# Performance work log

Measured on AMD Instinct MI355X. Metric: run time of the kernel, lower is better.

Reference implementation:

```python
import jax, jax.numpy as jnp
import numpy as np

N = 524288
EPS = 1e-5

def _ln(x, g, b):
    m = jnp.mean(x, axis=-1, keepdims=True)
    v = jnp.mean((x - m) ** 2, axis=-1, keepdims=True)
    return (x - m) * jax.lax.rsqrt(v + EPS) * g + b

def _blk(x, w1, g, b, w2, b2):
    # Linear(no bias) -> LayerNorm -> ReLU -> Linear(bias)
    return jax.nn.relu(_ln(x @ w1, g, b)) @ w2 + b2

def _lin_init(k, fin, fout):
    return jax.random.normal(k, (fin, fout), dtype=jnp.float32) * (1.0 / np.sqrt(fin))

def setup_inputs() -> dict:
    key = jax.random.key(0)
    ks = jax.random.split(key, 16)
    d = {
        'representation_128': jax.random.normal(ks[0], (N, 128), dtype=jnp.float32),
        'grasp_pose': jax.random.normal(ks[1], (N, 6), dtype=jnp.float32),
        'opening': jax.random.uniform(ks[2], (N, 1), dtype=jnp.float32),
        # key branch: 128 -> 64 (no bias) -> LN -> ReLU -> 32
        'kw1': _lin_init(ks[3], 128, 64), 'kg': jnp.ones(64), 'kb': jnp.zeros(64),
        'kw2': _lin_init(ks[4], 64, 32), 'kb2': jnp.zeros(32),
        # query branch: 6 -> 16 -> 32
        'qw1': _lin_init(ks[5], 6, 16), 'qg': jnp.ones(16), 'qb': jnp.zeros(16),
        'qw2': _lin_init(ks[6], 16, 32), 'qb2': jnp.zeros(32),
        # value branch: 1 -> 16 -> 32
        'vw1': _lin_init(ks[7], 1, 16), 'vg': jnp.ones(16), 'vb': jnp.zeros(16),
        'vw2': _lin_init(ks[8], 16, 32), 'vb2': jnp.zeros(32),
        # attention head: 32 -> 32 -> 16
        'aw1': _lin_init(ks[9], 32, 32), 'ag': jnp.ones(32), 'ab': jnp.zeros(32),
        'aw2': _lin_init(ks[10], 32, 16), 'ab2': jnp.zeros(16),
        # residuals: 135 -> 64 -> 32 -> 16 (two LN blocks, final Linear with bias)
        'rw1': _lin_init(ks[11], 135, 64), 'rg1': jnp.ones(64), 'rb1': jnp.zeros(64),
        'rw2': _lin_init(ks[12], 64, 32), 'rg2': jnp.ones(32), 'rb2': jnp.zeros(32),
        'rw3': _lin_init(ks[13], 32, 16), 'rb3': jnp.zeros(16),
        # get_value: 32 -> 16 -> 1
        'gw1': _lin_init(ks[14], 32, 16), 'gg': jnp.ones(16), 'gb': jnp.zeros(16),
        'gw2': _lin_init(ks[15], 16, 1), 'gb2': jnp.zeros(1),
    }
    return d

def reference(representation_128, grasp_pose, opening,
              kw1, kg, kb, kw2, kb2,
              qw1, qg, qb, qw2, qb2,
              vw1, vg, vb, vw2, vb2,
              aw1, ag, ab, aw2, ab2,
              rw1, rg1, rb1, rw2, rg2, rb2, rw3, rb3,
              gw1, gg, gb, gw2, gb2):
    # residual path on concat([rep, pose, opening]) -> [N,135]
    res_in = jnp.concatenate([representation_128, grasp_pose, opening], axis=-1)
    h = jax.nn.relu(_ln(res_in @ rw1, rg1, rb1))
    h = jax.nn.relu(_ln(h @ rw2, rg2, rb2))
    residuals = h @ rw3 + rb3                       # [N,16]
    key = _blk(representation_128, kw1, kg, kb, kw2, kb2)   # [N,32]
    query = _blk(grasp_pose, qw1, qg, qb, qw2, qb2)          # [N,32]
    value = _blk(opening, vw1, vg, vb, vw2, vb2)             # [N,32]
    att = jax.nn.softmax(query * key, axis=-1) * value       # [N,32]
    att = _blk(att, aw1, ag, ab, aw2, ab2)                   # [N,16]
    features = jnp.concatenate([att, residuals], axis=-1)    # [N,32]
    score = _blk(features, gw1, gg, gb, gw2, gb2)            # [N,1]
    return score
```

## Files before the change

### kernel.cpp

```cpp
#include <hip/hip_runtime.h>
#include <math.h>

#define LN_EPS 1e-5f

typedef float v2f  __attribute__((ext_vector_type(2)));
typedef float f32x4 __attribute__((ext_vector_type(4)));
typedef short s16x8 __attribute__((ext_vector_type(8)));

__device__ __forceinline__ v2f pf(v2f a, v2f b, v2f c) {
    return __builtin_elementwise_fma(a, b, c);
}
__device__ __forceinline__ v2f bc2(float s) { v2f r; r.x = s; r.y = s; return r; }
__device__ __forceinline__ v2f vmax2(v2f a, v2f b) {
    v2f r; r.x = fmaxf(a.x, b.x); r.y = fmaxf(a.y, b.y); return r;
}

__device__ __forceinline__ short f2bf(float f) {
    union { float f; unsigned u; } v; v.f = f;
    return (short)((v.u + 0x7fffu + ((v.u >> 16) & 1u)) >> 16);
}
__device__ __forceinline__ float bf2f(short s) {
    union { unsigned u; float f; } v; v.u = ((unsigned)(unsigned short)s) << 16;
    return v.f;
}

template<int D2>
__device__ __forceinline__ void ln_relu2(v2f (&v)[D2],
                                         const float* __restrict__ g,
                                         const float* __restrict__ b) {
    const float invD = 1.0f / (float)(2 * D2);
    v2f p0 = bc2(0.f), p1 = bc2(0.f), p2 = bc2(0.f), p3 = bc2(0.f);
#pragma unroll
    for (int i = 0; i < D2; i += 4) {
        p0 += v[i]; p1 += v[i + 1]; p2 += v[i + 2]; p3 += v[i + 3];
    }
    const v2f ps = (p0 + p1) + (p2 + p3);
    const float m = (ps.x + ps.y) * invD;
    const v2f mm = bc2(m);
    v2f q0 = bc2(0.f), q1 = bc2(0.f), q2 = bc2(0.f), q3 = bc2(0.f);
#pragma unroll
    for (int i = 0; i < D2; i += 4) {
        const v2f d0 = v[i] - mm, d1 = v[i + 1] - mm;
        const v2f d2 = v[i + 2] - mm, d3 = v[i + 3] - mm;
        q0 = pf(d0, d0, q0); q1 = pf(d1, d1, q1);
        q2 = pf(d2, d2, q2); q3 = pf(d3, d3, q3);
    }
    const v2f qs = (q0 + q1) + (q2 + q3);
    const float var = (qs.x + qs.y) * invD;
    const float rs = rsqrtf(var + LN_EPS);
    const v2f* g2 = (const v2f*)g;
    const v2f* b2 = (const v2f*)b;
#pragma unroll
    for (int i = 0; i < D2; ++i) {
        v2f t = pf((v[i] - mm) * rs, g2[i], b2[i]);
        v[i].x = fmaxf(t.x, 0.f);
        v[i].y = fmaxf(t.y, 0.f);
    }
}

template<int IN2, int OUT2>
__device__ __forceinline__ void mv2(const v2f (&x)[IN2],
                                    const float* __restrict__ W,
                                    v2f (&y)[OUT2]) {
    const v2f* W2 = (const v2f*)W;
#pragma unroll
    for (int j = 0; j < OUT2; ++j) y[j] = bc2(0.f);
#pragma unroll
    for (int k2 = 0; k2 < IN2; ++k2) {
        const v2f x0 = bc2(x[k2].x), x1 = bc2(x[k2].y);
#pragma unroll
        for (int j = 0; j < OUT2; ++j) {
            y[j] = pf(x0, W2[(2 * k2) * OUT2 + j], y[j]);
            y[j] = pf(x1, W2[(2 * k2 + 1) * OUT2 + j], y[j]);
        }
    }
}

template<int IN2, int OUT2>
__device__ __forceinline__ void mv2_bias(const v2f (&x)[IN2],
                                         const float* __restrict__ W,
                                         const float* __restrict__ bias,
                                         v2f (&y)[OUT2]) {
    const v2f* W2 = (const v2f*)W;
    const v2f* b2 = (const v2f*)bias;
#pragma unroll
    for (int j = 0; j < OUT2; ++j) y[j] = b2[j];
#pragma unroll
    for (int k2 = 0; k2 < IN2; ++k2) {
        const v2f x0 = bc2(x[k2].x), x1 = bc2(x[k2].y);
#pragma unroll
        for (int j = 0; j < OUT2; ++j) {
            y[j] = pf(x0, W2[(2 * k2) * OUT2 + j], y[j]);
            y[j] = pf(x1, W2[(2 * k2 + 1) * OUT2 + j], y[j]);
        }
    }
}

__global__ __launch_bounds__(256, 2) void opening_critic_stage(
    const float* __restrict__ rep,
    const float* __restrict__ kw1, const float* __restrict__ rw1,
    short* __restrict__ o1, short* __restrict__ o2, int nloc)
{
    __shared__ __align__(16) short scratch[4][64][72];

    const int tid  = threadIdx.x;
    const int wave = tid >> 6, lane = tid & 63;
    const int waveRow0 = blockIdx.x * 256 + wave * 64;
    const int myrow    = waveRow0 + lane;
    const int lm = lane & 15, quad = lane >> 4;

    s16x8 afr[4][4];
#pragma unroll
    for (int rt = 0; rt < 4; ++rt) {
        int arow = waveRow0 + rt * 16 + lm;
        if (arow >= nloc) arow = nloc - 1;
        const float* ap = rep + (size_t)arow * 128 + quad * 8;
#pragma unroll
        for (int kc = 0; kc < 4; ++kc) {
            const float4 x0 = *(const float4*)(ap + kc * 32);
            const float4 x1 = *(const float4*)(ap + kc * 32 + 4);
            s16x8 t;
            t[0] = f2bf(x0.x); t[1] = f2bf(x0.y); t[2] = f2bf(x0.z); t[3] = f2bf(x0.w);
            t[4] = f2bf(x1.x); t[5] = f2bf(x1.y); t[6] = f2bf(x1.z); t[7] = f2bf(x1.w);
            afr[rt][kc] = t;
        }
    }

#pragma unroll 1
    for (int w = 0; w < 2; ++w) {
        const float* __restrict__ W = w ? rw1 : kw1;
        short* __restrict__ O = w ? o2 : o1;

#pragma unroll
        for (int ct = 0; ct < 4; ++ct) {
            s16x8 bfr[4];
#pragma unroll
            for (int kc = 0; kc < 4; ++kc) {
                const float* wp = W + (size_t)(kc * 32 + quad * 8) * 64 + ct * 16 + lm;
                s16x8 t;
#pragma unroll
                for (int j = 0; j < 8; ++j) t[j] = f2bf(wp[j * 64]);
                bfr[kc] = t;
            }
#pragma unroll
            for (int rt = 0; rt < 4; ++rt) {
                f32x4 acc = (f32x4){0.f, 0.f, 0.f, 0.f};
#pragma unroll
                for (int kc = 0; kc < 4; ++kc)
                    acc = __builtin_amdgcn_mfma_f32_16x16x32_bf16(
                        afr[rt][kc], bfr[kc], acc, 0, 0, 0);
#pragma unroll
                for (int reg = 0; reg < 4; ++reg)
                    scratch[wave][rt * 16 + quad * 4 + reg][ct * 16 + lm] = f2bf(acc[reg]);
            }
        }

        asm volatile("s_waitcnt lgkmcnt(0)" ::: "memory");
        if (myrow < nloc) {
            const s16x8* sr = (const s16x8*)scratch[wave][lane];
            s16x8* dst = (s16x8*)(O + (size_t)myrow * 64);
#pragma unroll
            for (int i = 0; i < 8; ++i) dst[i] = sr[i];
        }
        asm volatile("s_waitcnt lgkmcnt(0)" ::: "memory");
    }
}

__global__ __launch_bounds__(256, 2) void opening_critic_tail(
    const short* __restrict__ o1, const short* __restrict__ o2,
    const float* __restrict__ pose, const float* __restrict__ opening,
    const float* __restrict__ kg,  const float* __restrict__ kb,
    const float* __restrict__ kw2, const float* __restrict__ kb2,
    const float* __restrict__ qw1, const float* __restrict__ qg,  const float* __restrict__ qb,
    const float* __restrict__ qw2, const float* __restrict__ qb2,
    const float* __restrict__ vw1, const float* __restrict__ vg,  const float* __restrict__ vb,
    const float* __restrict__ vw2, const float* __restrict__ vb2,
    const float* __restrict__ aw1, const float* __restrict__ ag,  const float* __restrict__ ab,
    const float* __restrict__ aw2, const float* __restrict__ ab2,
    const float* __restrict__ rw1, const float* __restrict__ rg1, const float* __restrict__ rb1,
    const float* __restrict__ rw2, const float* __restrict__ rg2, const float* __restrict__ rb2,
    const float* __restrict__ rw3, const float* __restrict__ rb3,
    const float* __restrict__ gw1, const float* __restrict__ gg,  const float* __restrict__ gb,
    const float* __restrict__ gw2, const float* __restrict__ gb2,
    float* __restrict__ out, int nloc)
{
    const int myrow = blockIdx.x * 256 + threadIdx.x;
    if (myrow >= nloc) return;

    float pv[6];
#pragma unroll
    for (int i = 0; i < 6; ++i) pv[i] = pose[(size_t)myrow * 6 + i];
    const float ov = opening[myrow];

    v2f key[16];
    {
        v2f ka[32];
        const s16x8* r1 = (const s16x8*)(o1 + (size_t)myrow * 64);
#pragma unroll
        for (int i = 0; i < 8; ++i) {
            const s16x8 t = r1[i];
#pragma unroll
            for (int j = 0; j < 4; ++j) {
                v2f u; u.x = bf2f(t[2 * j]); u.y = bf2f(t[2 * j + 1]);
                ka[i * 4 + j] = u;
            }
        }
        ln_relu2<32>(ka, kg, kb);
        mv2_bias<32, 16>(ka, kw2, kb2, key);
    }

    v2f s[16];
    {
        v2f q1[8];
        const v2f* qw1_2 = (const v2f*)qw1;
#pragma unroll
        for (int j = 0; j < 8; ++j) q1[j] = bc2(0.f);
#pragma unroll
        for (int k = 0; k < 6; ++k) {
            const v2f xv = bc2(pv[k]);
#pragma unroll
            for (int j = 0; j < 8; ++j) q1[j] = pf(xv, qw1_2[k * 8 + j], q1[j]);
        }
        ln_relu2<8>(q1, qg, qb);
        v2f query[16];
        mv2_bias<8, 16>(q1, qw2, qb2, query);
#pragma unroll
        for (int j = 0; j < 16; ++j) s[j] = query[j] * key[j];
    }

    float mx;
    {
        v2f t8[8];
#pragma unroll
        for (int j = 0; j < 8; ++j) t8[j] = vmax2(s[j], s[j + 8]);
        v2f t4a = vmax2(t8[0], t8[4]), t4b = vmax2(t8[1], t8[5]);
        v2f t4c = vmax2(t8[2], t8[6]), t4d = vmax2(t8[3], t8[7]);
        v2f t2 = vmax2(vmax2(t4a, t4b), vmax2(t4c, t4d));
        mx = fmaxf(t2.x, t2.y);
    }
    float sum;
    {
        v2f p0 = bc2(0.f), p1 = bc2(0.f), p2 = bc2(0.f), p3 = bc2(0.f);
#pragma unroll
        for (int j = 0; j < 16; j += 4) {
            s[j].x     = __expf(s[j].x - mx);     s[j].y     = __expf(s[j].y - mx);
            s[j + 1].x = __expf(s[j + 1].x - mx); s[j + 1].y = __expf(s[j + 1].y - mx);
            s[j + 2].x = __expf(s[j + 2].x - mx); s[j + 2].y = __expf(s[j + 2].y - mx);
            s[j + 3].x = __expf(s[j + 3].x - mx); s[j + 3].y = __expf(s[j + 3].y - mx);
            p0 += s[j]; p1 += s[j + 1]; p2 += s[j + 2]; p3 += s[j + 3];
        }
        const v2f ps = (p0 + p1) + (p2 + p3);
        sum = ps.x + ps.y;
    }
    const float inv = 1.0f / sum;

    s16x8 raw2[8];
    {
        const s16x8* r2 = (const s16x8*)(o2 + (size_t)myrow * 64);
#pragma unroll
        for (int i = 0; i < 8; ++i) raw2[i] = r2[i];
    }

    {
        v2f v1[8];
        const v2f* vw1_2 = (const v2f*)vw1;
        const v2f xo = bc2(ov);
#pragma unroll
        for (int j = 0; j < 8; ++j) v1[j] = xo * vw1_2[j];
        ln_relu2<8>(v1, vg, vb);
        v2f value[16];
        mv2_bias<8, 16>(v1, vw2, vb2, value);
#pragma unroll
        for (int j = 0; j < 16; ++j) s[j] = s[j] * inv * value[j];
    }

    v2f att[8];
    {
        v2f a1[16];
        mv2<16, 16>(s, aw1, a1);
        ln_relu2<16>(a1, ag, ab);
        mv2_bias<16, 8>(a1, aw2, ab2, att);
    }

    v2f residuals[8];
    {
        v2f ra[32];
#pragma unroll
        for (int i = 0; i < 8; ++i) {
            const s16x8 t = raw2[i];
#pragma unroll
            for (int j = 0; j < 4; ++j) {
                v2f u; u.x = bf2f(t[2 * j]); u.y = bf2f(t[2 * j + 1]);
                ra[i * 4 + j] = u;
            }
        }
#pragma unroll
        for (int kk = 0; kk < 6; ++kk) {
            const v2f* w = (const v2f*)(rw1 + (128 + kk) * 64);
            const v2f xv = bc2(pv[kk]);
#pragma unroll
            for (int j = 0; j < 32; ++j) ra[j] = pf(xv, w[j], ra[j]);
        }
        {
            const v2f* w = (const v2f*)(rw1 + 134 * 64);
            const v2f xo = bc2(ov);
#pragma unroll
            for (int j = 0; j < 32; ++j) ra[j] = pf(xo, w[j], ra[j]);
        }
        ln_relu2<32>(ra, rg1, rb1);
        v2f h2[16];
        mv2<32, 16>(ra, rw2, h2);
        ln_relu2<16>(h2, rg2, rb2);
        mv2_bias<16, 8>(h2, rw3, rb3, residuals);
    }

    float score;
    {
        v2f g1[8];
        const v2f* gw1_2 = (const v2f*)gw1;
#pragma unroll
        for (int j = 0; j < 8; ++j) g1[j] = bc2(0.f);
#pragma unroll
        for (int k2 = 0; k2 < 8; ++k2) {
            const v2f x0 = bc2(att[k2].x), x1 = bc2(att[k2].y);
#pragma unroll
            for (int j = 0; j < 8; ++j) {
                g1[j] = pf(x0, gw1_2[(2 * k2) * 8 + j], g1[j]);
                g1[j] = pf(x1, gw1_2[(2 * k2 + 1) * 8 + j], g1[j]);
            }
        }
#pragma unroll
        for (int k2 = 0; k2 < 8; ++k2) {
            const v2f x0 = bc2(residuals[k2].x), x1 = bc2(residuals[k2].y);
#pragma unroll
            for (int j = 0; j < 8; ++j) {
                g1[j] = pf(x0, gw1_2[(16 + 2 * k2) * 8 + j], g1[j]);
                g1[j] = pf(x1, gw1_2[(16 + 2 * k2 + 1) * 8 + j], g1[j]);
            }
        }
        ln_relu2<8>(g1, gg, gb);
        score = gb2[0];
        const v2f* gw2_2 = (const v2f*)gw2;
#pragma unroll
        for (int k = 0; k < 8; ++k) {
            score = fmaf(g1[k].x, gw2_2[k].x, score);
            score = fmaf(g1[k].y, gw2_2[k].y, score);
        }
    }

    out[myrow] = score;
}

extern "C" void kernel_launch(void* const* d_in, const int* in_sizes, int n_in,
                              void* d_out, int out_size, void* d_ws, size_t ws_size,
                              hipStream_t stream) {
    const float* rep     = (const float*)d_in[0];
    const float* pose    = (const float*)d_in[1];
    const float* opening = (const float*)d_in[2];
    const float* kw1 = (const float*)d_in[3];
    const float* kg  = (const float*)d_in[4];
    const float* kb  = (const float*)d_in[5];
    const float* kw2 = (const float*)d_in[6];
    const float* kb2 = (const float*)d_in[7];
    const float* qw1 = (const float*)d_in[8];
    const float* qg  = (const float*)d_in[9];
    const float* qb  = (const float*)d_in[10];
    const float* qw2 = (const float*)d_in[11];
    const float* qb2 = (const float*)d_in[12];
    const float* vw1 = (const float*)d_in[13];
    const float* vg  = (const float*)d_in[14];
    const float* vb  = (const float*)d_in[15];
    const float* vw2 = (const float*)d_in[16];
    const float* vb2 = (const float*)d_in[17];
    const float* aw1 = (const float*)d_in[18];
    const float* ag  = (const float*)d_in[19];
    const float* ab  = (const float*)d_in[20];
    const float* aw2 = (const float*)d_in[21];
    const float* ab2 = (const float*)d_in[22];
    const float* rw1 = (const float*)d_in[23];
    const float* rg1 = (const float*)d_in[24];
    const float* rb1 = (const float*)d_in[25];
    const float* rw2 = (const float*)d_in[26];
    const float* rg2 = (const float*)d_in[27];
    const float* rb2 = (const float*)d_in[28];
    const float* rw3 = (const float*)d_in[29];
    const float* rb3 = (const float*)d_in[30];
    const float* gw1 = (const float*)d_in[31];
    const float* gg  = (const float*)d_in[32];
    const float* gb  = (const float*)d_in[33];
    const float* gw2 = (const float*)d_in[34];
    const float* gb2 = (const float*)d_in[35];

    const int n = in_sizes[0] / 128;
    float* out = (float*)d_out;

    const size_t perRowBytes = 2 * 64 * sizeof(short);
    const long long cap = (long long)(ws_size / perRowBytes);
    int C;
    if (cap >= (long long)n) C = n;
    else {
        C = (int)((cap / 256) * 256);
        if (C < 256) C = 256;
    }
    short* o1 = (short*)d_ws;
    short* o2 = o1 + (size_t)C * 64;

    dim3 block(256);
    for (int r0 = 0; r0 < n; r0 += C) {
        const int nloc = (n - r0 < C) ? (n - r0) : C;
        dim3 grid((nloc + 255) / 256);
        hipLaunchKernelGGL(opening_critic_stage, grid, block, 0, stream,
                           rep + (size_t)r0 * 128, kw1, rw1, o1, o2, nloc);
        hipLaunchKernelGGL(opening_critic_tail, grid, block, 0, stream,
                           o1, o2, pose + (size_t)r0 * 6, opening + r0,
                           kg, kb, kw2, kb2,
                           qw1, qg, qb, qw2, qb2,
                           vw1, vg, vb, vw2, vb2,
                           aw1, ag, ab, aw2, ab2,
                           rw1, rg1, rb1, rw2, rg2, rb2, rw3, rb3,
                           gw1, gg, gb, gw2, gb2,
                           out + r0, nloc);
    }
}
```

Baseline: 683.2 us.

## Fuse LN and second-layer matmuls into MFMA stage, halving intermediate buffers

The stage kernel now applies LayerNorm+ReLU to the first-layer outputs and runs the second linear layers (kw2, rw2) with bf16 MFMA through LDS, including the pose/opening contributions to the residual path. The intermediates written to workspace shrink from 64 to 32 bf16 per row per branch, and the tail kernel loses the 64->32 scalar matvecs. This targets both HBM traffic between kernels and scalar FMA work, at the cost of more bf16 rounding of activations and extra LDS round trips in the stage kernel.

New measurement: 554.8 us. -18.8%, faster.

```diff
diff --git a/kernel.cpp b/kernel.cpp
--- a/kernel.cpp
+++ b/kernel.cpp
@@ -96,9 +96,76 @@
     }
 }
 
+
+__device__ __forceinline__ void mm1(const s16x8 (&afr)[4][4],
+                                    const float* __restrict__ W1,
+                                    int lm, int quad,
+                                    short (*__restrict__ sc)[72]) {
+#pragma unroll
+    for (int ct = 0; ct < 4; ++ct) {
+        s16x8 bfr[4];
+#pragma unroll
+        for (int kc = 0; kc < 4; ++kc) {
+            const float* wp = W1 + (size_t)(kc * 32 + quad * 8) * 64 + ct * 16 + lm;
+            s16x8 t;
+#pragma unroll
+            for (int j = 0; j < 8; ++j) t[j] = f2bf(wp[j * 64]);
+            bfr[kc] = t;
+        }
+#pragma unroll
+        for (int rt = 0; rt < 4; ++rt) {
+            f32x4 acc = (f32x4){0.f, 0.f, 0.f, 0.f};
+#pragma unroll
+            for (int kc = 0; kc < 4; ++kc)
+                acc = __builtin_amdgcn_mfma_f32_16x16x32_bf16(
+                    afr[rt][kc], bfr[kc], acc, 0, 0, 0);
+#pragma unroll
+            for (int reg = 0; reg < 4; ++reg)
+                sc[rt * 16 + quad * 4 + reg][ct * 16 + lm] = f2bf(acc[reg]);
+        }
+    }
+}
+
+__device__ __forceinline__ void mm2(const float* __restrict__ W2,
+                                    int lm, int quad,
+                                    short (*__restrict__ sc)[72]) {
+    s16x8 a2[4][2];
+#pragma unroll
+    for (int rt = 0; rt < 4; ++rt)
+#pragma unroll
+        for (int kc = 0; kc < 2; ++kc)
+            a2[rt][kc] = *(const s16x8*)&sc[rt * 16 + lm][kc * 32 + quad * 8];
+    asm volatile("s_waitcnt lgkmcnt(0)" ::: "memory");
+#pragma unroll
+    for (int ct = 0; ct < 2; ++ct) {
+        s16x8 b2[2];
+#pragma unroll
+        for (int kc = 0; kc < 2; ++kc) {
+            const float* wp = W2 + (size_t)(kc * 32 + quad * 8) * 32 + ct * 16 + lm;
+            s16x8 t;
+#pragma unroll
+            for (int j = 0; j < 8; ++j) t[j] = f2bf(wp[j * 32]);
+            b2[kc] = t;
+        }
+#pragma unroll
+        for (int rt = 0; rt < 4; ++rt) {
+            f32x4 acc = (f32x4){0.f, 0.f, 0.f, 0.f};
+            acc = __builtin_amdgcn_mfma_f32_16x16x32_bf16(a2[rt][0], b2[0], acc, 0, 0, 0);
+            acc = __builtin_amdgcn_mfma_f32_16x16x32_bf16(a2[rt][1], b2[1], acc, 0, 0, 0);
+#pragma unroll
+            for (int reg = 0; reg < 4; ++reg)
+                sc[rt * 16 + quad * 4 + reg][ct * 16 + lm] = f2bf(acc[reg]);
+        }
+    }
+}
+
 __global__ __launch_bounds__(256, 2) void opening_critic_stage(
-    const float* __restrict__ rep,
-    const float* __restrict__ kw1, const float* __restrict__ rw1,
+    const float* __restrict__ rep, const float* __restrict__ pose,
+    const float* __restrict__ opening,
+    const float* __restrict__ kw1, const float* __restrict__ kg,
+    const float* __restrict__ kb,  const float* __restrict__ kw2,
+    const float* __restrict__ rw1, const float* __restrict__ rg1,
+    const float* __restrict__ rb1, const float* __restrict__ rw2,
     short* __restrict__ o1, short* __restrict__ o2, int nloc)
 {
     __shared__ __align__(16) short scratch[4][64][72];
@@ -107,7 +174,14 @@
     const int wave = tid >> 6, lane = tid & 63;
     const int waveRow0 = blockIdx.x * 256 + wave * 64;
     const int myrow    = waveRow0 + lane;
+    const int rowc     = (myrow < nloc) ? myrow : (nloc - 1);
     const int lm = lane & 15, quad = lane >> 4;
+    short (*sc)[72] = scratch[wave];
+
+    float pv[6];
+#pragma unroll
+    for (int i = 0; i < 6; ++i) pv[i] = pose[(size_t)rowc * 6 + i];
+    const float ov = opening[rowc];
 
     s16x8 afr[4][4];
 #pragma unroll
@@ -126,59 +200,128 @@
         }
     }
 
-#pragma unroll 1
-    for (int w = 0; w < 2; ++w) {
-        const float* __restrict__ W = w ? rw1 : kw1;
-        short* __restrict__ O = w ? o2 : o1;
-
-#pragma unroll
-        for (int ct = 0; ct < 4; ++ct) {
-            s16x8 bfr[4];
-#pragma unroll
-            for (int kc = 0; kc < 4; ++kc) {
-                const float* wp = W + (size_t)(kc * 32 + quad * 8) * 64 + ct * 16 + lm;
-                s16x8 t;
-#pragma unroll
-                for (int j = 0; j < 8; ++j) t[j] = f2bf(wp[j * 64]);
-                bfr[kc] = t;
+    mm1(afr, kw1, lm, quad, sc);
+    asm volatile("s_waitcnt lgkmcnt(0)" ::: "memory");
+    {
+        s16x8 rowb[8];
+        const s16x8* sr = (const s16x8*)sc[lane];
+#pragma unroll
+        for (int i = 0; i < 8; ++i) rowb[i] = sr[i];
+        asm volatile("s_waitcnt lgkmcnt(0)" ::: "memory");
+
+        v2f p0 = bc2(0.f), p1 = bc2(0.f), p2 = bc2(0.f), p3 = bc2(0.f);
+#pragma unroll
+        for (int i = 0; i < 8; ++i) {
+            v2f u0, u1, u2, u3;
+            u0.x = bf2f(rowb[i][0]); u0.y = bf2f(rowb[i][1]);
+            u1.x = bf2f(rowb[i][2]); u1.y = bf2f(rowb[i][3]);
+            u2.x = bf2f(rowb[i][4]); u2.y = bf2f(rowb[i][5]);
+            u3.x = bf2f(rowb[i][6]); u3.y = bf2f(rowb[i][7]);
+            p0 += u0; p1 += u1; p2 += u2; p3 += u3;
+        }
+        const v2f ps = (p0 + p1) + (p2 + p3);
+        const float m = (ps.x + ps.y) * (1.0f / 64.0f);
+        const v2f mm = bc2(m);
+        v2f q0 = bc2(0.f), q1 = bc2(0.f), q2 = bc2(0.f), q3 = bc2(0.f);
+#pragma unroll
+        for (int i = 0; i < 8; ++i) {
+            v2f u0, u1, u2, u3;
+            u0.x = bf2f(rowb[i][0]); u0.y = bf2f(rowb[i][1]);
+            u1.x = bf2f(rowb[i][2]); u1.y = bf2f(rowb[i][3]);
+            u2.x = bf2f(rowb[i][4]); u2.y = bf2f(rowb[i][5]);
+            u3.x = bf2f(rowb[i][6]); u3.y = bf2f(rowb[i][7]);
+            const v2f d0 = u0 - mm, d1 = u1 - mm, d2 = u2 - mm, d3 = u3 - mm;
+            q0 = pf(d0, d0, q0); q1 = pf(d1, d1, q1);
+            q2 = pf(d2, d2, q2); q3 = pf(d3, d3, q3);
+        }
+        const v2f qs = (q0 + q1) + (q2 + q3);
+        const float rs = rsqrtf((qs.x + qs.y) * (1.0f / 64.0f) + LN_EPS);
+
+        s16x8* dl = (s16x8*)sc[lane];
+#pragma unroll
+        for (int i = 0; i < 8; ++i) {
+            s16x8 h;
+#pragma unroll
+            for (int e = 0; e < 8; ++e) {
+                const float x = bf2f(rowb[i][e]);
+                const float t = fmaf((x - m) * rs, kg[i * 8 + e], kb[i * 8 + e]);
+                h[e] = f2bf(fmaxf(t, 0.f));
             }
-#pragma unroll
-            for (int rt = 0; rt < 4; ++rt) {
-                f32x4 acc = (f32x4){0.f, 0.f, 0.f, 0.f};
-#pragma unroll
-                for (int kc = 0; kc < 4; ++kc)
-                    acc = __builtin_amdgcn_mfma_f32_16x16x32_bf16(
-                        afr[rt][kc], bfr[kc], acc, 0, 0, 0);
-#pragma unroll
-                for (int reg = 0; reg < 4; ++reg)
-                    scratch[wave][rt * 16 + quad * 4 + reg][ct * 16 + lm] = f2bf(acc[reg]);
+            dl[i] = h;
+        }
+    }
+    asm volatile("s_waitcnt lgkmcnt(0)" ::: "memory");
+    mm2(kw2, lm, quad, sc);
+    asm volatile("s_waitcnt lgkmcnt(0)" ::: "memory");
+    if (myrow < nloc) {
+        const s16x8* s2 = (const s16x8*)sc[lane];
+        s16x8* dst = (s16x8*)(o1 + (size_t)myrow * 32);
+#pragma unroll
+        for (int i = 0; i < 4; ++i) dst[i] = s2[i];
+    }
+    asm volatile("s_waitcnt lgkmcnt(0)" ::: "memory");
+
+    mm1(afr, rw1, lm, quad, sc);
+    asm volatile("s_waitcnt lgkmcnt(0)" ::: "memory");
+    {
+        v2f row[32];
+        const short* sr = sc[lane];
+#pragma unroll
+        for (int c = 0; c < 32; ++c) {
+            v2f t; t.x = bf2f(sr[2 * c]); t.y = bf2f(sr[2 * c + 1]);
+            row[c] = t;
+        }
+        asm volatile("s_waitcnt lgkmcnt(0)" ::: "memory");
+
+#pragma unroll
+        for (int kk = 0; kk < 6; ++kk) {
+            const v2f* w = (const v2f*)(rw1 + (size_t)(128 + kk) * 64);
+            const v2f xv = bc2(pv[kk]);
+#pragma unroll
+            for (int j = 0; j < 32; ++j) row[j] = pf(xv, w[j], row[j]);
+        }
+        {
+            const v2f* w = (const v2f*)(rw1 + (size_t)134 * 64);
+            const v2f xo = bc2(ov);
+#pragma unroll
+            for (int j = 0; j < 32; ++j) row[j] = pf(xo, w[j], row[j]);
+        }
+        ln_relu2<32>(row, rg1, rb1);
+
+        s16x8* dl = (s16x8*)sc[lane];
+#pragma unroll
+        for (int i = 0; i < 8; ++i) {
+            s16x8 h;
+#pragma unroll
+            for (int j = 0; j < 4; ++j) {
+                h[2 * j]     = f2bf(row[i * 4 + j].x);
+                h[2 * j + 1] = f2bf(row[i * 4 + j].y);
             }
-        }
-
-        asm volatile("s_waitcnt lgkmcnt(0)" ::: "memory");
-        if (myrow < nloc) {
-            const s16x8* sr = (const s16x8*)scratch[wave][lane];
-            s16x8* dst = (s16x8*)(O + (size_t)myrow * 64);
-#pragma unroll
-            for (int i = 0; i < 8; ++i) dst[i] = sr[i];
-        }
-        asm volatile("s_waitcnt lgkmcnt(0)" ::: "memory");
+            dl[i] = h;
+        }
+    }
+    asm volatile("s_waitcnt lgkmcnt(0)" ::: "memory");
+    mm2(rw2, lm, quad, sc);
+    asm volatile("s_waitcnt lgkmcnt(0)" ::: "memory");
+    if (myrow < nloc) {
+        const s16x8* s2 = (const s16x8*)sc[lane];
+        s16x8* dst = (s16x8*)(o2 + (size_t)myrow * 32);
+#pragma unroll
+        for (int i = 0; i < 4; ++i) dst[i] = s2[i];
     }
 }
 
 __global__ __launch_bounds__(256, 2) void opening_critic_tail(
     const short* __restrict__ o1, const short* __restrict__ o2,
     const float* __restrict__ pose, const float* __restrict__ opening,
-    const float* __restrict__ kg,  const float* __restrict__ kb,
-    const float* __restrict__ kw2, const float* __restrict__ kb2,
+    const float* __restrict__ kb2,
     const float* __restrict__ qw1, const float* __restrict__ qg,  const float* __restrict__ qb,
     const float* __restrict__ qw2, const float* __restrict__ qb2,
     const float* __restrict__ vw1, const float* __restrict__ vg,  const float* __restrict__ vb,
     const float* __restrict__ vw2, const float* __restrict__ vb2,
     const float* __restrict__ aw1, const float* __restrict__ ag,  const float* __restrict__ ab,
     const float* __restrict__ aw2, const float* __restrict__ ab2,
-    const float* __restrict__ rw1, const float* __restrict__ rg1, const float* __restrict__ rb1,
-    const float* __restrict__ rw2, const float* __restrict__ rg2, const float* __restrict__ rb2,
+    const float* __restrict__ rg2, const float* __restrict__ rb2,
     const float* __restrict__ rw3, const float* __restrict__ rb3,
     const float* __restrict__ gw1, const float* __restrict__ gg,  const float* __restrict__ gb,
     const float* __restrict__ gw2, const float* __restrict__ gb2,
@@ -194,19 +337,17 @@
 
     v2f key[16];
     {
-        v2f ka[32];
-        const s16x8* r1 = (const s16x8*)(o1 + (size_t)myrow * 64);
-#pragma unroll
-        for (int i = 0; i < 8; ++i) {
+        const s16x8* r1 = (const s16x8*)(o1 + (size_t)myrow * 32);
+        const v2f* b2 = (const v2f*)kb2;
+#pragma unroll
+        for (int i = 0; i < 4; ++i) {
             const s16x8 t = r1[i];
 #pragma unroll
             for (int j = 0; j < 4; ++j) {
                 v2f u; u.x = bf2f(t[2 * j]); u.y = bf2f(t[2 * j + 1]);
-                ka[i * 4 + j] = u;
+                key[i * 4 + j] = u + b2[i * 4 + j];
             }
         }
-        ln_relu2<32>(ka, kg, kb);
-        mv2_bias<32, 16>(ka, kw2, kb2, key);
     }
 
     v2f s[16];
@@ -254,11 +395,11 @@
     }
     const float inv = 1.0f / sum;
 
-    s16x8 raw2[8];
-    {
-        const s16x8* r2 = (const s16x8*)(o2 + (size_t)myrow * 64);
-#pragma unroll
-        for (int i = 0; i < 8; ++i) raw2[i] = r2[i];
+    s16x8 rawh[4];
+    {
+        const s16x8* r2 = (const s16x8*)(o2 + (size_t)myrow * 32);
+#pragma unroll
+        for (int i = 0; i < 4; ++i) rawh[i] = r2[i];
     }
 
     {
@@ -284,32 +425,16 @@
 
     v2f residuals[8];
     {
-        v2f ra[32];
-#pragma unroll
-        for (int i = 0; i < 8; ++i) {
-            const s16x8 t = raw2[i];
+        v2f h2[16];
+#pragma unroll
+        for (int i = 0; i < 4; ++i) {
+            const s16x8 t = rawh[i];
 #pragma unroll
             for (int j = 0; j < 4; ++j) {
                 v2f u; u.x = bf2f(t[2 * j]); u.y = bf2f(t[2 * j + 1]);
-                ra[i * 4 + j] = u;
+                h2[i * 4 + j] = u;
             }
         }
-#pragma unroll
-        for (int kk = 0; kk < 6; ++kk) {
-            const v2f* w = (const v2f*)(rw1 + (128 + kk) * 64);
-            const v2f xv = bc2(pv[kk]);
-#pragma unroll
-            for (int j = 0; j < 32; ++j) ra[j] = pf(xv, w[j], ra[j]);
-        }
-        {
-            const v2f* w = (const v2f*)(rw1 + 134 * 64);
-            const v2f xo = bc2(ov);
-#pragma unroll
-            for (int j = 0; j < 32; ++j) ra[j] = pf(xo, w[j], ra[j]);
-        }
-        ln_relu2<32>(ra, rg1, rb1);
-        v2f h2[16];
-        mv2<32, 16>(ra, rw2, h2);
         ln_relu2<16>(h2, rg2, rb2);
         mv2_bias<16, 8>(h2, rw3, rb3, residuals);
     }
@@ -394,7 +519,7 @@
     const int n = in_sizes[0] / 128;
     float* out = (float*)d_out;
 
-    const size_t perRowBytes = 2 * 64 * sizeof(short);
+    const size_t perRowBytes = 2 * 32 * sizeof(short);
     const long long cap = (long long)(ws_size / perRowBytes);
     int C;
     if (cap >= (long long)n) C = n;
@@ -403,21 +528,24 @@
         if (C < 256) C = 256;
     }
     short* o1 = (short*)d_ws;
-    short* o2 = o1 + (size_t)C * 64;
+    short* o2 = o1 + (size_t)C * 32;
 
     dim3 block(256);
     for (int r0 = 0; r0 < n; r0 += C) {
         const int nloc = (n - r0 < C) ? (n - r0) : C;
         dim3 grid((nloc + 255) / 256);
         hipLaunchKernelGGL(opening_critic_stage, grid, block, 0, stream,
-                           rep + (size_t)r0 * 128, kw1, rw1, o1, o2, nloc);
+                           rep + (size_t)r0 * 128, pose + (size_t)r0 * 6, opening + r0,
+                           kw1, kg, kb, kw2,
+                           rw1, rg1, rb1, rw2,
+                           o1, o2, nloc);
         hipLaunchKernelGGL(opening_critic_tail, grid, block, 0, stream,
                            o1, o2, pose + (size_t)r0 * 6, opening + r0,
-                           kg, kb, kw2, kb2,
+                           kb2,
                            qw1, qg, qb, qw2, qb2,
                            vw1, vg, vb, vw2, vb2,
                            aw1, ag, ab, aw2, ab2,
-                           rw1, rg1, rb1, rw2, rg2, rb2, rw3, rb3,
+                           rg2, rb2, rw3, rb3,
                            gw1, gg, gb, gw2, gb2,
                            out + r0, nloc);
     }
```
